# Kernel optimization log

Hardware: AMD Instinct MI355X
Metric: run time of the kernel (lower is better)

## Reference

```python
import jax, jax.numpy as jnp
import numpy as np

D_MODEL = 768
N_HEADS = 4
HEAD_DIM = D_MODEL // N_HEADS


def setup_inputs() -> dict:
    key = jax.random.key(0)
    ks = jax.random.split(key, 9)
    B, S = 4, 2048
    scale = 1.0 / np.sqrt(D_MODEL)
    inputs = jax.random.normal(ks[0], (B, S, D_MODEL), dtype=jnp.float32)
    # Linear weights stored as [in, out] for x @ W + b
    Wq = jax.random.normal(ks[1], (D_MODEL, D_MODEL), dtype=jnp.float32) * scale
    bq = jnp.zeros((D_MODEL,), dtype=jnp.float32)
    Wk = jax.random.normal(ks[2], (D_MODEL, D_MODEL), dtype=jnp.float32) * scale
    bk = jnp.zeros((D_MODEL,), dtype=jnp.float32)
    Wv = jax.random.normal(ks[3], (D_MODEL, D_MODEL), dtype=jnp.float32) * scale
    bv = jnp.zeros((D_MODEL,), dtype=jnp.float32)
    Wo = jax.random.normal(ks[4], (D_MODEL, D_MODEL), dtype=jnp.float32) * scale
    bo = jnp.zeros((D_MODEL,), dtype=jnp.float32)
    return {"inputs": inputs, "Wq": Wq, "bq": bq, "Wk": Wk, "bk": bk,
            "Wv": Wv, "bv": bv, "Wo": Wo, "bo": bo}


def reference(inputs, Wq, bq, Wk, bk, Wv, bv, Wo, bo):
    B, S, _ = inputs.shape
    H, Dh = N_HEADS, HEAD_DIM
    # projections -> [B, H, S, Dh]
    def split_heads(x):
        return x.reshape(B, S, H, Dh).transpose(0, 2, 1, 3)
    Q = split_heads(inputs @ Wq + bq)
    K = split_heads(inputs @ Wk + bk)
    V = split_heads(inputs @ Wv + bv)
    scores = jnp.einsum('bhqd,bhkd->bhqk', Q, K) / jnp.sqrt(jnp.float32(Dh))
    causal = jnp.tril(jnp.ones((S, S), dtype=bool))  # True = keep
    scores = jnp.where(causal, scores, -jnp.inf)
    weights = jax.nn.softmax(scores, axis=-1)
    # dropout is identity in eval mode
    ctx = jnp.einsum('bhqk,bhkd->bhqd', weights, V)
    ctx = ctx.transpose(0, 2, 1, 3).reshape(B, S, H * Dh)
    return ctx @ Wo + bo
```

## Files before the change

kernel.cpp:

```cpp
#include <hip/hip_runtime.h>
#include <hip/hip_bf16.h>
#include <cstddef>

typedef __attribute__((ext_vector_type(8))) short short8;
typedef __attribute__((ext_vector_type(4))) float f32x4;
typedef __attribute__((ext_vector_type(16))) float f32x16;
typedef __attribute__((ext_vector_type(4))) unsigned short u16x4;

#define D_MODEL 768
#define N_HEADS 4
#define HEAD_DIM 192
#define BATCH 4
#define SEQ 2048
#define M_ROWS (BATCH*SEQ)

__device__ __forceinline__ short f2bf(float f) {
  union { float f; unsigned u; } v; v.f = f;
  unsigned r = v.u + 0x7FFFu + ((v.u >> 16) & 1u);
  return (short)(r >> 16);
}

__device__ __forceinline__ float fexp2(float x) {
  return __builtin_amdgcn_exp2f(x);
}

__device__ __forceinline__ void gl_lds16(const void* g, void* l) {
  __builtin_amdgcn_global_load_lds(
      (const __attribute__((address_space(1))) void*)g,
      (__attribute__((address_space(3))) void*)l, 16, 0, 0);
}

__global__ __launch_bounds__(256) void cast_kernel(const float* __restrict__ src,
                                                   short* __restrict__ dst, int n8) {
  int i = blockIdx.x * 256 + threadIdx.x;
  if (i >= n8) return;
  const float4* s = (const float4*)src;
  float4 a = s[2 * i], b = s[2 * i + 1];
  short8 o;
  o[0] = f2bf(a.x); o[1] = f2bf(a.y); o[2] = f2bf(a.z); o[3] = f2bf(a.w);
  o[4] = f2bf(b.x); o[5] = f2bf(b.y); o[6] = f2bf(b.z); o[7] = f2bf(b.w);
  *(short8*)(dst + (size_t)i * 8) = o;
}

__global__ __launch_bounds__(256) void wtrans4(const float* __restrict__ W0,
                                               const float* __restrict__ W1,
                                               const float* __restrict__ W2,
                                               const float* __restrict__ W3,
                                               short* __restrict__ Wqkvt,
                                               short* __restrict__ Wot) {
  __shared__ float tile[32][33];
  int z = blockIdx.z;
  const float* W = z == 0 ? W0 : (z == 1 ? W1 : (z == 2 ? W2 : W3));
  short* Wt = z < 3 ? (Wqkvt + (size_t)z * 768 * 768) : Wot;
  int k0 = blockIdx.x * 32, n0 = blockIdx.y * 32;
  int tc = threadIdx.x & 31, tr = threadIdx.x >> 5;
#pragma unroll
  for (int i = 0; i < 4; i++)
    tile[tr + i * 8][tc] = W[(size_t)(k0 + tr + i * 8) * D_MODEL + n0 + tc];
  __syncthreads();
#pragma unroll
  for (int i = 0; i < 4; i++)
    Wt[(size_t)(n0 + tr + i * 8) * D_MODEL + k0 + tc] = f2bf(tile[tc][tr + i * 8]);
}

template <int MODE>
__global__ __launch_bounds__(256, 4) void gemm_bf16(const short* __restrict__ A,
                                                    const short* __restrict__ Wt,
                                                    const float* __restrict__ b0,
                                                    const float* __restrict__ b1,
                                                    const float* __restrict__ b2,
                                                    short* __restrict__ oQ,
                                                    short* __restrict__ oK,
                                                    short* __restrict__ oV,
                                                    float* __restrict__ oF,
                                                    int N, int NB) {
  __shared__ short As[128 * 64];
  __shared__ short Bs[128 * 64];
  const int K = 768;
  const int lid = blockIdx.x;
  const int nlid = (lid & 7) * ((int)gridDim.x >> 3) + (lid >> 3);
  const int m0 = (nlid / NB) * 128, n0 = (nlid % NB) * 128;
  const int t = threadIdx.x, lane = t & 63, w = t >> 6;
  const int wr = w >> 1, wc = w & 1, lr = lane & 15, lg = lane >> 4;

  f32x4 acc[4][4] = {};

  for (int k0 = 0; k0 < K; k0 += 64) {
#pragma unroll
    for (int i = 0; i < 4; i++) {
      int id = w * 4 + i;
      int row = id * 8 + (lane >> 3);
      int cc = (lane & 7) ^ (row & 7);
      gl_lds16(A + (size_t)(m0 + row) * K + k0 + cc * 8, As + id * 512);
      gl_lds16(Wt + (size_t)(n0 + row) * K + k0 + cc * 8, Bs + id * 512);
    }
    __syncthreads();
#pragma unroll
    for (int kb = 0; kb < 2; kb++) {
      short8 a[4], b[4];
#pragma unroll
      for (int m = 0; m < 4; m++) {
        int row = wr * 64 + m * 16 + lr;
        a[m] = *(const short8*)&As[row * 64 + (((kb * 4 + lg) ^ (row & 7)) << 3)];
      }
#pragma unroll
      for (int n = 0; n < 4; n++) {
        int row = wc * 64 + n * 16 + lr;
        b[n] = *(const short8*)&Bs[row * 64 + (((kb * 4 + lg) ^ (row & 7)) << 3)];
      }
#pragma unroll
      for (int m = 0; m < 4; m++)
#pragma unroll
        for (int n = 0; n < 4; n++)
          acc[m][n] = __builtin_amdgcn_mfma_f32_16x16x32_bf16(a[m], b[n], acc[m][n], 0, 0, 0);
    }
    __syncthreads();
  }

  if (MODE == 0) {
#pragma unroll
    for (int m = 0; m < 4; m++)
#pragma unroll
      for (int n = 0; n < 4; n++) {
        int col = n0 + wc * 64 + n * 16 + lr;
        float bv = b0[col];
#pragma unroll
        for (int r = 0; r < 4; r++) {
          int row = m0 + wr * 64 + m * 16 + lg * 4 + r;
          oF[(size_t)row * N + col] = acc[m][n][r] + bv;
        }
      }
  } else {
    const int bb = m0 >> 11;
#pragma unroll
    for (int m = 0; m < 4; m++) {
      int s0 = (m0 & (SEQ - 1)) + wr * 64 + m * 16 + lg * 4;
#pragma unroll
      for (int n = 0; n < 4; n++) {
        int col = n0 + wc * 64 + n * 16 + lr;
        int seg = col / 768;
        int d = col - seg * 768;
        int h = d / HEAD_DIM, dd = d - h * HEAD_DIM;
        int bh = bb * N_HEADS + h;
        float bv = (seg == 0 ? b0 : (seg == 1 ? b1 : b2))[d];
        if (seg < 2) {
          short* dst = seg == 0 ? oQ : oK;
#pragma unroll
          for (int r = 0; r < 4; r++)
            dst[((size_t)bh * SEQ + s0 + r) * HEAD_DIM + dd] = f2bf(acc[m][n][r] + bv);
        } else {
          u16x4 pk;
#pragma unroll
          for (int r = 0; r < 4; r++) pk[r] = (unsigned short)f2bf(acc[m][n][r] + bv);
          *(u16x4*)&oV[((size_t)bh * HEAD_DIM + dd) * SEQ + s0] = pk;
        }
      }
    }
  }
}

__device__ __forceinline__ void stage_kv(const short* Kp, const short* Vp, int kbase,
                                         short* KsB, short* VsB, int w, int lane) {
#pragma unroll
  for (int i = 0; i < 6; i++) {
    int id = w * 6 + i;
    int o16 = id * 64 + lane;
    int row = o16 / 24, cc0 = o16 - row * 24;
    int cc = cc0 ^ (row & 7);
    gl_lds16(Kp + (size_t)(kbase + row) * HEAD_DIM + cc * 8, KsB + id * 512);
  }
#pragma unroll
  for (int i = 0; i < 6; i++) {
    int id = w * 6 + i;
    int o16 = id * 64 + lane;
    int row = o16 >> 3, cc = (o16 & 7) ^ (row & 7);
    gl_lds16(Vp + (size_t)row * SEQ + kbase + cc * 8, VsB + id * 512);
  }
}

__global__ __launch_bounds__(256, 2) void attn_kernel(const short* __restrict__ Q,
                                                      const short* __restrict__ Kg,
                                                      const short* __restrict__ Vt,
                                                      short* __restrict__ ctx) {
  __shared__ short smem[64 * 192 + 192 * 64];
  __shared__ float mlbuf[128];
  short* Ks = smem;
  short* Vs = smem + 64 * 192;
  float* obuf = (float*)smem;

  const int i = blockIdx.x;
  const int bh = ((i & 7) << 1) | (i >> 8);
  const int qt = (i >> 3) & 31;

  const int b = bh >> 2, head = bh & 3;
  const short* Qp = Q + (size_t)bh * SEQ * HEAD_DIM;
  const short* Kp = Kg + (size_t)bh * SEQ * HEAD_DIM;
  const short* Vp = Vt + (size_t)bh * HEAD_DIM * SEQ;
  const int t = threadIdx.x, lane = t & 63, w = t >> 6;
  const int wq = w >> 1, wk = w & 1;
  const int l31 = lane & 31, hl = lane >> 5;
  const float scale2 = 0.07216878364870322f * 1.4426950408889634f;

  const int nkb = qt + 1;
  const int q0w = qt * 64 + wq * 32;
  const int qlane = q0w + l31;

  short8 qf[12];
#pragma unroll
  for (int c = 0; c < 12; c++)
    qf[c] = *(const short8*)&Qp[(size_t)qlane * HEAD_DIM + c * 16 + hl * 8];

  f32x16 oacc[6];
#pragma unroll
  for (int d = 0; d < 6; d++) oacc[d] = 0.f;
  float m = -3.0e38f, lsum = 0.f;

  for (int kb = 0; kb < nkb; kb++) {
    const int kbase = kb * 64;
    stage_kv(Kp, Vp, kbase, Ks, Vs, w, lane);
    asm volatile("s_waitcnt vmcnt(0)" ::: "memory");
    __builtin_amdgcn_s_barrier();
    asm volatile("" ::: "memory");

    if (kbase + wk * 32 <= q0w + 31) {
      f32x16 sacc = 0.f, sacc2 = 0.f;
      const int krow = wk * 32 + l31;
      const int krb = krow * 192;
      const int kswz = (krow & 7) << 3;
      __builtin_amdgcn_s_setprio(1);
#pragma unroll
      for (int c = 0; c < 12; c += 2) {
        short8 kf0 = *(const short8*)&Ks[krb + ((c * 16 + hl * 8) ^ kswz)];
        short8 kf1 = *(const short8*)&Ks[krb + (((c + 1) * 16 + hl * 8) ^ kswz)];
        sacc = __builtin_amdgcn_mfma_f32_32x32x16_bf16(kf0, qf[c], sacc, 0, 0, 0);
        sacc2 = __builtin_amdgcn_mfma_f32_32x32x16_bf16(kf1, qf[c + 1], sacc2, 0, 0, 0);
      }
      __builtin_amdgcn_s_setprio(0);

      float s[16];
      const bool need_mask = (kbase + wk * 32 + 31) > q0w;
      const int kb0 = kbase + wk * 32 + 4 * hl;
#pragma unroll
      for (int r = 0; r < 16; r++) {
        float v = (sacc[r] + sacc2[r]) * scale2;
        if (need_mask) {
          int kg = kb0 + (r & 3) + 8 * (r >> 2);
          if (kg > qlane) v = -3.0e38f;
        }
        s[r] = v;
      }
      float mx = s[0];
#pragma unroll
      for (int r = 1; r < 16; r++) mx = fmaxf(mx, s[r]);
      mx = fmaxf(mx, __shfl_xor(mx, 32, 64));
      if (!__all(mx <= m + 8.0f)) {
        float mn = fmaxf(m, mx);
        float al = fexp2(m - mn);
        m = mn;
        lsum *= al;
#pragma unroll
        for (int d = 0; d < 6; d++) oacc[d] *= al;
      }
      float pr[16];
      float rs = 0.f;
#pragma unroll
      for (int r = 0; r < 16; r++) {
        pr[r] = fexp2(s[r] - m);
        rs += pr[r];
      }
      rs += __shfl_xor(rs, 32, 64);
      lsum += rs;

      unsigned pk[8], ex[8];
#pragma unroll
      for (int j = 0; j < 8; j++) {
        unsigned r0;
        asm("v_cvt_pk_bf16_f32 %0, %1, %2" : "=v"(r0) : "v"(pr[2 * j]), "v"(pr[2 * j + 1]));
        pk[j] = r0;
      }
#pragma unroll
      for (int j = 0; j < 8; j++) ex[j] = __shfl_xor((int)pk[j], 32, 64);
      union { unsigned u[4]; short8 s8; } f0, f1;
      f0.u[0] = hl ? ex[2] : pk[0];
      f0.u[1] = hl ? ex[3] : pk[1];
      f0.u[2] = hl ? pk[2] : ex[0];
      f0.u[3] = hl ? pk[3] : ex[1];
      f1.u[0] = hl ? ex[6] : pk[4];
      f1.u[1] = hl ? ex[7] : pk[5];
      f1.u[2] = hl ? pk[6] : ex[4];
      f1.u[3] = hl ? pk[7] : ex[5];

      __builtin_amdgcn_s_setprio(1);
#pragma unroll
      for (int db = 0; db < 6; db++) {
        const int vrow = db * 32 + l31;
        const int vrb = vrow * 64;
        const int vswz = (vrow & 7) << 3;
        short8 va = *(const short8*)&Vs[vrb + ((wk * 32 + hl * 8) ^ vswz)];
        oacc[db] = __builtin_amdgcn_mfma_f32_32x32x16_bf16(va, f0.s8, oacc[db], 0, 0, 0);
        short8 vb = *(const short8*)&Vs[vrb + ((wk * 32 + 16 + hl * 8) ^ vswz)];
        oacc[db] = __builtin_amdgcn_mfma_f32_32x32x16_bf16(vb, f1.s8, oacc[db], 0, 0, 0);
      }
      __builtin_amdgcn_s_setprio(0);
    }
    asm volatile("" ::: "memory");
    __builtin_amdgcn_s_barrier();
  }

  __syncthreads();
  if (wk == 1) {
    if (lane < 32) {
      mlbuf[wq * 64 + lane] = m;
      mlbuf[wq * 64 + 32 + lane] = lsum;
    }
#pragma unroll
    for (int db = 0; db < 6; db++)
#pragma unroll
      for (int g = 0; g < 4; g++) {
        int d = db * 32 + 8 * g + 4 * hl;
        f32x4 vv;
        vv[0] = oacc[db][4 * g];
        vv[1] = oacc[db][4 * g + 1];
        vv[2] = oacc[db][4 * g + 2];
        vv[3] = oacc[db][4 * g + 3];
        *(f32x4*)&obuf[(wq * 32 + l31) * 192 + (d ^ ((l31 & 7) << 2))] = vv;
      }
  }
  __syncthreads();
  if (wk == 0) {
    float m1 = mlbuf[wq * 64 + l31];
    float l1 = mlbuf[wq * 64 + 32 + l31];
    float ms = fmaxf(m, m1);
    float a0 = fexp2(m - ms), a1 = fexp2(m1 - ms);
    float lt = lsum * a0 + l1 * a1;
    float rl = 1.0f / lt;
#pragma unroll
    for (int db = 0; db < 6; db++)
#pragma unroll
      for (int g = 0; g < 4; g++) {
        int d = db * 32 + 8 * g + 4 * hl;
        f32x4 rd = *(const f32x4*)&obuf[(wq * 32 + l31) * 192 + (d ^ ((l31 & 7) << 2))];
        u16x4 pkk;
#pragma unroll
        for (int r2 = 0; r2 < 4; r2++) {
          float v = (oacc[db][4 * g + r2] * a0 + rd[r2] * a1) * rl;
          pkk[r2] = (unsigned short)f2bf(v);
        }
        *(u16x4*)&ctx[((size_t)b * SEQ + qlane) * D_MODEL + head * HEAD_DIM + d] = pkk;
      }
  }
}

extern "C" void kernel_launch(void* const* d_in, const int* in_sizes, int n_in,
                              void* d_out, int out_size, void* d_ws, size_t ws_size,
                              hipStream_t stream) {
  const float* X  = (const float*)d_in[0];
  const float* Wq = (const float*)d_in[1];
  const float* bq = (const float*)d_in[2];
  const float* Wk = (const float*)d_in[3];
  const float* bk = (const float*)d_in[4];
  const float* Wv = (const float*)d_in[5];
  const float* bv = (const float*)d_in[6];
  const float* Wo = (const float*)d_in[7];
  const float* bo = (const float*)d_in[8];

  char* ws = (char*)d_ws;
  const size_t XB = (size_t)M_ROWS * D_MODEL * 2;
  const size_t WQKV = (size_t)3 * D_MODEL * D_MODEL * 2;
  const size_t WB = (size_t)D_MODEL * D_MODEL * 2;

  short* Xb    = (short*)(ws);
  short* Wqkvt = (short*)(ws + XB);
  short* Wot   = (short*)(ws + XB + WQKV);
  short* Qb    = (short*)(ws + XB + WQKV + WB + 12288);
  short* Kb    = (short*)(ws + XB + WQKV + WB + 12288 + XB);
  short* Vtb   = (short*)(ws + XB + WQKV + WB + 12288 + 2 * XB);
  short* Cb    = (short*)(ws + XB + WQKV + WB + 12288 + 3 * XB);

  const int n8x = M_ROWS * D_MODEL / 8;
  cast_kernel<<<(n8x + 255) / 256, 256, 0, stream>>>(X, Xb, n8x);
  wtrans4<<<dim3(24, 24, 4), 256, 0, stream>>>(Wq, Wk, Wv, Wo, Wqkvt, Wot);

  gemm_bf16<1><<<1152, 256, 0, stream>>>(Xb, Wqkvt, bq, bk, bv,
                                         Qb, Kb, Vtb, nullptr, 2304, 18);

  attn_kernel<<<512, 256, 0, stream>>>(Qb, Kb, Vtb, Cb);

  gemm_bf16<0><<<384, 256, 0, stream>>>(Cb, Wot, bo, bo, bo,
                                        nullptr, nullptr, nullptr, (float*)d_out, 768, 6);
}
```

Baseline: 149.8 us.

## Split long causal query tiles across two blocks with a merge kernel

The attention grid grows to 768 blocks. The 16 longest query tiles per batch-head have their key range split in half across two blocks, each writing unnormalized fp32 partial outputs plus max and sum to workspace. A new merge kernel combines the partials with log-sum-exp rescaling and writes bf16 context. The aim is to balance the causal triangle's uneven per-tile work across CUs, at the cost of extra fp32 partial traffic and one more launch.

```diff
diff --git a/kernel.cpp b/kernel.cpp
--- a/kernel.cpp
+++ b/kernel.cpp
@@ -181,7 +181,9 @@
 __global__ __launch_bounds__(256, 2) void attn_kernel(const short* __restrict__ Q,
                                                       const short* __restrict__ Kg,
                                                       const short* __restrict__ Vt,
-                                                      short* __restrict__ ctx) {
+                                                      short* __restrict__ ctx,
+                                                      float* __restrict__ Pbuf,
+                                                      float* __restrict__ Mbuf) {
   __shared__ short smem[64 * 192 + 192 * 64];
   __shared__ float mlbuf[128];
   short* Ks = smem;
@@ -189,8 +191,19 @@
   float* obuf = (float*)smem;
 
   const int i = blockIdx.x;
-  const int bh = ((i & 7) << 1) | (i >> 8);
-  const int qt = (i >> 3) & 31;
+  const int c = i & 255, s = i >> 8;
+  const int bh = c & 15, tt = c >> 4;
+  int qt, kb0, kcnt, split, half;
+  if (s == 2) {
+    qt = tt; kb0 = 0; kcnt = tt + 1; split = 0; half = 0;
+  } else {
+    qt = 31 - tt;
+    int nk = 32 - tt, h = nk >> 1;
+    int first = ((s ^ (tt & 1)) == 0);
+    kb0 = first ? 0 : h;
+    kcnt = first ? h : nk - h;
+    split = 1; half = first ? 0 : 1;
+  }
 
   const int b = bh >> 2, head = bh & 3;
   const short* Qp = Q + (size_t)bh * SEQ * HEAD_DIM;
@@ -201,22 +214,21 @@
   const int l31 = lane & 31, hl = lane >> 5;
   const float scale2 = 0.07216878364870322f * 1.4426950408889634f;
 
-  const int nkb = qt + 1;
   const int q0w = qt * 64 + wq * 32;
   const int qlane = q0w + l31;
 
   short8 qf[12];
 #pragma unroll
-  for (int c = 0; c < 12; c++)
-    qf[c] = *(const short8*)&Qp[(size_t)qlane * HEAD_DIM + c * 16 + hl * 8];
+  for (int cq = 0; cq < 12; cq++)
+    qf[cq] = *(const short8*)&Qp[(size_t)qlane * HEAD_DIM + cq * 16 + hl * 8];
 
   f32x16 oacc[6];
 #pragma unroll
   for (int d = 0; d < 6; d++) oacc[d] = 0.f;
   float m = -3.0e38f, lsum = 0.f;
 
-  for (int kb = 0; kb < nkb; kb++) {
-    const int kbase = kb * 64;
+  for (int kbi = kb0; kbi < kb0 + kcnt; kbi++) {
+    const int kbase = kbi * 64;
     stage_kv(Kp, Vp, kbase, Ks, Vs, w, lane);
     asm volatile("s_waitcnt vmcnt(0)" ::: "memory");
     __builtin_amdgcn_s_barrier();
@@ -229,29 +241,29 @@
       const int kswz = (krow & 7) << 3;
       __builtin_amdgcn_s_setprio(1);
 #pragma unroll
-      for (int c = 0; c < 12; c += 2) {
-        short8 kf0 = *(const short8*)&Ks[krb + ((c * 16 + hl * 8) ^ kswz)];
-        short8 kf1 = *(const short8*)&Ks[krb + (((c + 1) * 16 + hl * 8) ^ kswz)];
-        sacc = __builtin_amdgcn_mfma_f32_32x32x16_bf16(kf0, qf[c], sacc, 0, 0, 0);
-        sacc2 = __builtin_amdgcn_mfma_f32_32x32x16_bf16(kf1, qf[c + 1], sacc2, 0, 0, 0);
+      for (int cq = 0; cq < 12; cq += 2) {
+        short8 kf0 = *(const short8*)&Ks[krb + ((cq * 16 + hl * 8) ^ kswz)];
+        short8 kf1 = *(const short8*)&Ks[krb + (((cq + 1) * 16 + hl * 8) ^ kswz)];
+        sacc = __builtin_amdgcn_mfma_f32_32x32x16_bf16(kf0, qf[cq], sacc, 0, 0, 0);
+        sacc2 = __builtin_amdgcn_mfma_f32_32x32x16_bf16(kf1, qf[cq + 1], sacc2, 0, 0, 0);
       }
       __builtin_amdgcn_s_setprio(0);
 
-      float s[16];
+      float sv[16];
       const bool need_mask = (kbase + wk * 32 + 31) > q0w;
-      const int kb0 = kbase + wk * 32 + 4 * hl;
+      const int kr0 = kbase + wk * 32 + 4 * hl;
 #pragma unroll
       for (int r = 0; r < 16; r++) {
         float v = (sacc[r] + sacc2[r]) * scale2;
         if (need_mask) {
-          int kg = kb0 + (r & 3) + 8 * (r >> 2);
+          int kg = kr0 + (r & 3) + 8 * (r >> 2);
           if (kg > qlane) v = -3.0e38f;
         }
-        s[r] = v;
-      }
-      float mx = s[0];
-#pragma unroll
-      for (int r = 1; r < 16; r++) mx = fmaxf(mx, s[r]);
+        sv[r] = v;
+      }
+      float mx = sv[0];
+#pragma unroll
+      for (int r = 1; r < 16; r++) mx = fmaxf(mx, sv[r]);
       mx = fmaxf(mx, __shfl_xor(mx, 32, 64));
       if (!__all(mx <= m + 8.0f)) {
         float mn = fmaxf(m, mx);
@@ -265,7 +277,7 @@
       float rs = 0.f;
 #pragma unroll
       for (int r = 0; r < 16; r++) {
-        pr[r] = fexp2(s[r] - m);
+        pr[r] = fexp2(sv[r] - m);
         rs += pr[r];
       }
       rs += __shfl_xor(rs, 32, 64);
@@ -333,21 +345,72 @@
     float ms = fmaxf(m, m1);
     float a0 = fexp2(m - ms), a1 = fexp2(m1 - ms);
     float lt = lsum * a0 + l1 * a1;
-    float rl = 1.0f / lt;
-#pragma unroll
-    for (int db = 0; db < 6; db++)
-#pragma unroll
-      for (int g = 0; g < 4; g++) {
-        int d = db * 32 + 8 * g + 4 * hl;
-        f32x4 rd = *(const f32x4*)&obuf[(wq * 32 + l31) * 192 + (d ^ ((l31 & 7) << 2))];
-        u16x4 pkk;
-#pragma unroll
-        for (int r2 = 0; r2 < 4; r2++) {
-          float v = (oacc[db][4 * g + r2] * a0 + rd[r2] * a1) * rl;
-          pkk[r2] = (unsigned short)f2bf(v);
+    const int row = wq * 32 + l31;
+    if (!split) {
+      float rl = 1.0f / lt;
+#pragma unroll
+      for (int db = 0; db < 6; db++)
+#pragma unroll
+        for (int g = 0; g < 4; g++) {
+          int d = db * 32 + 8 * g + 4 * hl;
+          f32x4 rd = *(const f32x4*)&obuf[row * 192 + (d ^ ((l31 & 7) << 2))];
+          u16x4 pkk;
+#pragma unroll
+          for (int r2 = 0; r2 < 4; r2++) {
+            float v = (oacc[db][4 * g + r2] * a0 + rd[r2] * a1) * rl;
+            pkk[r2] = (unsigned short)f2bf(v);
+          }
+          *(u16x4*)&ctx[((size_t)b * SEQ + qlane) * D_MODEL + head * HEAD_DIM + d] = pkk;
         }
-        *(u16x4*)&ctx[((size_t)b * SEQ + qlane) * D_MODEL + head * HEAD_DIM + d] = pkk;
-      }
+    } else {
+      const int sidx = (bh * 16 + (qt - 16)) * 2 + half;
+      float* P = Pbuf + ((size_t)sidx * 64 + row) * 192;
+      float* M = Mbuf + sidx * 128;
+      if (hl == 0) { M[row] = ms; M[64 + row] = lt; }
+#pragma unroll
+      for (int db = 0; db < 6; db++)
+#pragma unroll
+        for (int g = 0; g < 4; g++) {
+          int d = db * 32 + 8 * g + 4 * hl;
+          f32x4 rd = *(const f32x4*)&obuf[row * 192 + (d ^ ((l31 & 7) << 2))];
+          f32x4 vv;
+#pragma unroll
+          for (int r2 = 0; r2 < 4; r2++)
+            vv[r2] = oacc[db][4 * g + r2] * a0 + rd[r2] * a1;
+          *(f32x4*)&P[d] = vv;
+        }
+    }
+  }
+}
+
+__global__ __launch_bounds__(256) void attn_merge(const float* __restrict__ Pbuf,
+                                                  const float* __restrict__ Mbuf,
+                                                  short* __restrict__ ctx) {
+  const int blk = blockIdx.x;
+  const int bh = blk >> 4, qx = blk & 15, qt = 16 + qx;
+  const int b = bh >> 2, head = bh & 3;
+  const int base = (bh * 16 + qx) * 2;
+  const float* M0 = Mbuf + (size_t)base * 128;
+  const float* M1 = M0 + 128;
+  const float* P0 = Pbuf + (size_t)base * 64 * 192;
+  const float* P1 = P0 + 64 * 192;
+  const int t = threadIdx.x;
+  const int row = t & 63, cg = t >> 6;
+  float m0 = M0[row], l0 = M0[64 + row];
+  float m1 = M1[row], l1 = M1[64 + row];
+  float ms = fmaxf(m0, m1);
+  float a0 = fexp2(m0 - ms), a1 = fexp2(m1 - ms);
+  float rl = 1.0f / (l0 * a0 + l1 * a1);
+  const int q = qt * 64 + row;
+#pragma unroll
+  for (int j = 0; j < 12; j++) {
+    int d = cg * 48 + j * 4;
+    f32x4 v0 = *(const f32x4*)&P0[row * 192 + d];
+    f32x4 v1 = *(const f32x4*)&P1[row * 192 + d];
+    u16x4 o;
+#pragma unroll
+    for (int r = 0; r < 4; r++) o[r] = (unsigned short)f2bf((v0[r] * a0 + v1[r] * a1) * rl);
+    *(u16x4*)&ctx[((size_t)b * SEQ + q) * D_MODEL + head * HEAD_DIM + d] = o;
   }
 }
 
@@ -376,6 +439,9 @@
   short* Kb    = (short*)(ws + XB + WQKV + WB + 12288 + XB);
   short* Vtb   = (short*)(ws + XB + WQKV + WB + 12288 + 2 * XB);
   short* Cb    = (short*)(ws + XB + WQKV + WB + 12288 + 3 * XB);
+  float* Pbuf  = (float*)(ws + XB + WQKV + WB + 12288 + 4 * XB);
+  float* Mbuf  = (float*)(ws + XB + WQKV + WB + 12288 + 4 * XB +
+                          (size_t)512 * 64 * 192 * 4);
 
   const int n8x = M_ROWS * D_MODEL / 8;
   cast_kernel<<<(n8x + 255) / 256, 256, 0, stream>>>(X, Xb, n8x);
@@ -384,7 +450,8 @@
   gemm_bf16<1><<<1152, 256, 0, stream>>>(Xb, Wqkvt, bq, bk, bv,
                                          Qb, Kb, Vtb, nullptr, 2304, 18);
 
-  attn_kernel<<<512, 256, 0, stream>>>(Qb, Kb, Vtb, Cb);
+  attn_kernel<<<768, 256, 0, stream>>>(Qb, Kb, Vtb, Cb, Pbuf, Mbuf);
+  attn_merge<<<256, 256, 0, stream>>>(Pbuf, Mbuf, Cb);
 
   gemm_bf16<0><<<384, 256, 0, stream>>>(Cb, Wot, bo, bo, bo,
                                         nullptr, nullptr, nullptr, (float*)d_out, 768, 6);
```

New measurement: 149.9 us. Within noise of the previous version (+0.1%).

## Fold softmax scale into Q projection, reorder attention blocks, tree reductions

Applied to the files above, without the earlier changes.

Folds the 1/sqrt(Dh)*log2(e) softmax scale into the Q projection epilogue, so the attention inner loop no longer multiplies every score. Remaps block indices so the longest causal query tiles (highest qt) launch first across all heads, for better load balance. Replaces the serial max and sum chains with tree reductions to shorten dependency chains. Applying the scale before bf16 rounding changes numerics slightly.

```diff
diff --git a/kernel.cpp b/kernel.cpp
--- a/kernel.cpp
+++ b/kernel.cpp
@@ -13,6 +13,7 @@
 #define BATCH 4
 #define SEQ 2048
 #define M_ROWS (BATCH*SEQ)
+#define QSCALE 0.10411754f
 
 __device__ __forceinline__ short f2bf(float f) {
   union { float f; unsigned u; } v; v.f = f;
@@ -145,9 +146,10 @@
         float bv = (seg == 0 ? b0 : (seg == 1 ? b1 : b2))[d];
         if (seg < 2) {
           short* dst = seg == 0 ? oQ : oK;
+          float qs = seg == 0 ? QSCALE : 1.0f;
 #pragma unroll
           for (int r = 0; r < 4; r++)
-            dst[((size_t)bh * SEQ + s0 + r) * HEAD_DIM + dd] = f2bf(acc[m][n][r] + bv);
+            dst[((size_t)bh * SEQ + s0 + r) * HEAD_DIM + dd] = f2bf((acc[m][n][r] + bv) * qs);
         } else {
           u16x4 pk;
 #pragma unroll
@@ -189,8 +191,9 @@
   float* obuf = (float*)smem;
 
   const int i = blockIdx.x;
-  const int bh = ((i & 7) << 1) | (i >> 8);
-  const int qt = (i >> 3) & 31;
+  int bh, qt;
+  if (i < 256) { bh = i & 15; qt = 31 - (i >> 4); }
+  else         { int j = i - 256; bh = j & 15; qt = j >> 4; }
 
   const int b = bh >> 2, head = bh & 3;
   const short* Qp = Q + (size_t)bh * SEQ * HEAD_DIM;
@@ -199,7 +202,6 @@
   const int t = threadIdx.x, lane = t & 63, w = t >> 6;
   const int wq = w >> 1, wk = w & 1;
   const int l31 = lane & 31, hl = lane >> 5;
-  const float scale2 = 0.07216878364870322f * 1.4426950408889634f;
 
   const int nkb = qt + 1;
   const int q0w = qt * 64 + wq * 32;
@@ -237,21 +239,23 @@
       }
       __builtin_amdgcn_s_setprio(0);
 
-      float s[16];
+      float sv[16];
       const bool need_mask = (kbase + wk * 32 + 31) > q0w;
       const int kb0 = kbase + wk * 32 + 4 * hl;
 #pragma unroll
       for (int r = 0; r < 16; r++) {
-        float v = (sacc[r] + sacc2[r]) * scale2;
+        float v = sacc[r] + sacc2[r];
         if (need_mask) {
           int kg = kb0 + (r & 3) + 8 * (r >> 2);
           if (kg > qlane) v = -3.0e38f;
         }
-        s[r] = v;
-      }
-      float mx = s[0];
-#pragma unroll
-      for (int r = 1; r < 16; r++) mx = fmaxf(mx, s[r]);
+        sv[r] = v;
+      }
+      float ma = fmaxf(fmaxf(sv[0], sv[1]), fmaxf(sv[2], sv[3]));
+      float mb = fmaxf(fmaxf(sv[4], sv[5]), fmaxf(sv[6], sv[7]));
+      float mc = fmaxf(fmaxf(sv[8], sv[9]), fmaxf(sv[10], sv[11]));
+      float md = fmaxf(fmaxf(sv[12], sv[13]), fmaxf(sv[14], sv[15]));
+      float mx = fmaxf(fmaxf(ma, mb), fmaxf(mc, md));
       mx = fmaxf(mx, __shfl_xor(mx, 32, 64));
       if (!__all(mx <= m + 8.0f)) {
         float mn = fmaxf(m, mx);
@@ -262,12 +266,13 @@
         for (int d = 0; d < 6; d++) oacc[d] *= al;
       }
       float pr[16];
-      float rs = 0.f;
-#pragma unroll
-      for (int r = 0; r < 16; r++) {
-        pr[r] = fexp2(s[r] - m);
-        rs += pr[r];
-      }
+#pragma unroll
+      for (int r = 0; r < 16; r++) pr[r] = fexp2(sv[r] - m);
+      float sa = (pr[0] + pr[1]) + (pr[2] + pr[3]);
+      float sb = (pr[4] + pr[5]) + (pr[6] + pr[7]);
+      float sc = (pr[8] + pr[9]) + (pr[10] + pr[11]);
+      float sd = (pr[12] + pr[13]) + (pr[14] + pr[15]);
+      float rs = (sa + sb) + (sc + sd);
       rs += __shfl_xor(rs, 32, 64);
       lsum += rs;
 
```

Result: faster. 141.5 us (-5.6%).
